# Performance work log

Measured on AMD Instinct MI355X. Metric: run time of the kernel, lower is better.

## Reference

```python
import jax, jax.numpy as jnp
import numpy as np

DIM = 512
NUM_HEADS = 8
HEAD_DIM = DIM // NUM_HEADS
EPS = 1e-12  # F.normalize default eps


def _l2norm(x):
    # F.normalize: x / max(||x||_2, eps) along last dim
    n = jnp.sqrt(jnp.sum(x * x, axis=-1, keepdims=True))
    return x / jnp.maximum(n, EPS)


def setup_inputs() -> dict:
    key = jax.random.key(0)
    ks = jax.random.split(key, 7)
    B, N, K = 8, 4096, 256
    scale = 1.0 / np.sqrt(DIM)
    return {
        "X_flat": jax.random.normal(ks[0], (B, N, DIM), jnp.float32),
        "S_tokens": jax.random.normal(ks[1], (B, K, DIM), jnp.float32),
        "Wq": jax.random.normal(ks[2], (DIM, DIM), jnp.float32) * scale,
        "Wk": jax.random.normal(ks[3], (DIM, DIM), jnp.float32) * scale,
        "Wv": jax.random.normal(ks[4], (DIM, DIM), jnp.float32) * scale,
        "Wo": jax.random.normal(ks[5], (DIM, DIM), jnp.float32) * scale,
        "temperature": jnp.ones((NUM_HEADS, 1, 1), jnp.float32),
    }


def reference(X_flat, S_tokens, Wq, Wk, Wv, Wo, temperature):
    B, N, C = X_flat.shape
    K = S_tokens.shape[1]
    H, D = NUM_HEADS, HEAD_DIM
    # torch Linear: y = x @ W.T
    q = (X_flat @ Wq.T).reshape(B, N, H, D).transpose(0, 2, 1, 3)   # (B,H,N,D)
    k = (S_tokens @ Wk.T).reshape(B, K, H, D).transpose(0, 2, 1, 3)  # (B,H,K,D)
    v = (S_tokens @ Wv.T).reshape(B, K, H, D).transpose(0, 2, 1, 3)  # (B,H,K,D)
    q = _l2norm(q)
    k = _l2norm(k)
    attn = jnp.einsum('bhnd,bhkd->bhnk', q, k) * temperature  # temperature (H,1,1) broadcasts
    attn = jax.nn.softmax(attn, axis=-1)
    out = jnp.einsum('bhnk,bhkd->bhnd', attn, v)
    out = out.transpose(0, 2, 1, 3).reshape(B, N, C)
    out = out @ Wo.T
    return X_flat + out
```

## Files before the change

kernel.cpp:

```cpp
#include <hip/hip_runtime.h>
#include <hip/hip_bf16.h>


typedef __bf16 bf16;
typedef __attribute__((ext_vector_type(8))) __bf16 bf16x8;
typedef __attribute__((ext_vector_type(4))) float f32x4;

#if __has_builtin(__builtin_amdgcn_exp2f)
#define EXP2(x) __builtin_amdgcn_exp2f(x)
#else
#define EXP2(x) exp2f(x)
#endif

__device__ __forceinline__ void gload_lds16(const void* g, void* l) {
  __builtin_amdgcn_global_load_lds(
      (__attribute__((address_space(1))) void*)g,
      (__attribute__((address_space(3))) void*)l, 16, 0, 0);
}

__device__ __forceinline__ unsigned pack2(float a, float b) {
  unsigned short x = __builtin_bit_cast(unsigned short, (bf16)a);
  unsigned short y = __builtin_bit_cast(unsigned short, (bf16)b);
  return (unsigned)x | ((unsigned)y << 16);
}

__global__ __launch_bounds__(256) void cvt_all(
    const float* __restrict__ X, const float* __restrict__ S,
    const float* __restrict__ Wq, const float* __restrict__ Wk,
    const float* __restrict__ Wv, const float* __restrict__ Wo,
    bf16* __restrict__ Xb, bf16* __restrict__ Sb, bf16* __restrict__ Wqb,
    bf16* __restrict__ Wkb, bf16* __restrict__ Wvb, bf16* __restrict__ Wob) {
  int i = blockIdx.x * 256 + threadIdx.x;
  const float* src;
  bf16* dst;
  int r;
  if (i < 2097152) {
    src = X; dst = Xb; r = i;
  } else if (i < 2228224) {
    src = S; dst = Sb; r = i - 2097152;
  } else {
    int j = i - 2228224;
    int w = j >> 15;
    r = j & 32767;
    src = (w == 0) ? Wq : (w == 1) ? Wk : (w == 2) ? Wv : Wo;
    dst = (w == 0) ? Wqb : (w == 1) ? Wkb : (w == 2) ? Wvb : Wob;
  }
  float4 a = *(const float4*)(src + (size_t)r * 8);
  float4 b = *(const float4*)(src + (size_t)r * 8 + 4);
  uint4 v;
  v.x = pack2(a.x, a.y);
  v.y = pack2(a.z, a.w);
  v.z = pack2(b.x, b.y);
  v.w = pack2(b.z, b.w);
  *(uint4*)(dst + (size_t)r * 8) = v;
}

__global__ __launch_bounds__(256) void proj_all(
    const bf16* __restrict__ Xb, const bf16* __restrict__ Sb,
    const bf16* __restrict__ Wqb, const bf16* __restrict__ Wkb,
    const bf16* __restrict__ Wvb, const float* __restrict__ temp,
    bf16* __restrict__ Q, bf16* __restrict__ Kn, bf16* __restrict__ Vt) {
  __shared__ __align__(16) char smem[49152];

  const int lg = (blockIdx.x & 7) * 144 + (blockIdx.x >> 3);

  const bf16* A;
  const bf16* W;
  int m0, kind;
  if (lg < 1024) {
    kind = 0; A = Xb; W = Wqb; m0 = (lg >> 2) * 128;
  } else if (lg < 1088) {
    kind = 1; A = Sb; W = Wkb; m0 = ((lg - 1024) >> 2) * 128;
  } else {
    kind = 2; A = Sb; W = Wvb; m0 = ((lg - 1088) >> 2) * 128;
  }
  const int n0 = (lg & 3) * 128;

  const int tid = threadIdx.x;
  const int wid = tid >> 6, lane = tid & 63;
  const int wr = wid >> 1, wc = wid & 1;
  const int g = lane >> 4, c16 = lane & 15;
  const int r0 = tid >> 2, cc0 = tid & 3;
  const int r1 = (256 + tid) >> 2, cc1 = tid & 3;
  const int dst0 = (tid & ~63) * 16, dst1 = (256 + (tid & ~63)) * 16;

  f32x4 acc[4][4] = {};

#define PSTAGE(kb, buf)                                                     \
  {                                                                         \
    char* as = smem + (buf) * 8192;                                         \
    char* bs = smem + 24576 + (buf) * 8192;                                 \
    gload_lds16(A + (size_t)(m0 + r0) * 512 + (kb) + cc0 * 8, as + dst0);   \
    gload_lds16(A + (size_t)(m0 + r1) * 512 + (kb) + cc1 * 8, as + dst1);   \
    gload_lds16(W + (size_t)(n0 + r0) * 512 + (kb) + cc0 * 8, bs + dst0);   \
    gload_lds16(W + (size_t)(n0 + r1) * 512 + (kb) + cc1 * 8, bs + dst1);   \
  }

#define PCOMPUTE(buf)                                                       \
  {                                                                         \
    const bf16* as = (const bf16*)(smem + (buf) * 8192);                    \
    const bf16* bs = (const bf16*)(smem + 24576 + (buf) * 8192);            \
    bf16x8 af[4], bfr[4];                                                   \
    _Pragma("unroll") for (int mi = 0; mi < 4; ++mi) af[mi] =               \
        *(const bf16x8*)(as + (wr * 64 + mi * 16 + c16) * 32 + g * 8);      \
    _Pragma("unroll") for (int ni = 0; ni < 4; ++ni) bfr[ni] =              \
        *(const bf16x8*)(bs + (wc * 64 + ni * 16 + c16) * 32 + g * 8);      \
    _Pragma("unroll") for (int mi = 0; mi < 4; ++mi)                        \
        _Pragma("unroll") for (int ni = 0; ni < 4; ++ni) acc[mi][ni] =      \
            __builtin_amdgcn_mfma_f32_16x16x32_bf16(af[mi], bfr[ni],        \
                                                    acc[mi][ni], 0, 0, 0);  \
  }

  PSTAGE(0, 0);
  PSTAGE(32, 1);
  int bufc = 0;
  for (int t = 0; t < 14; ++t) {
    int bufn = bufc + 2;
    if (bufn >= 3) bufn -= 3;
    PSTAGE((t + 2) * 32, bufn);
    asm volatile("s_waitcnt vmcnt(8)" ::: "memory");
    __builtin_amdgcn_s_barrier();
    PCOMPUTE(bufc);
    __builtin_amdgcn_s_barrier();
    if (++bufc == 3) bufc = 0;
  }
  asm volatile("s_waitcnt vmcnt(4)" ::: "memory");
  __builtin_amdgcn_s_barrier();
  PCOMPUTE(bufc);
  __builtin_amdgcn_s_barrier();
  if (++bufc == 3) bufc = 0;
  asm volatile("s_waitcnt vmcnt(0)" ::: "memory");
  __builtin_amdgcn_s_barrier();
  PCOMPUTE(bufc);

  __syncthreads();

  if (kind != 2) {
    bf16* C = (kind == 0) ? Q : Kn;
    const float sc =
        (kind == 0) ? temp[(n0 + wc * 64) >> 6] * 1.44269504088896f : 1.0f;
    char* eps = smem + wid * 8192;
#pragma unroll
    for (int mi = 0; mi < 4; ++mi) {
      float ss[4];
#pragma unroll
      for (int j = 0; j < 4; ++j) {
        float s = 0.f;
#pragma unroll
        for (int ni = 0; ni < 4; ++ni) {
          float v = acc[mi][ni][j];
          s += v * v;
        }
        ss[j] = s;
      }
#pragma unroll
      for (int msk = 1; msk < 16; msk <<= 1)
#pragma unroll
        for (int j = 0; j < 4; ++j) ss[j] += __shfl_xor(ss[j], msk, 64);
      float inv[4];
#pragma unroll
      for (int j = 0; j < 4; ++j)
        inv[j] = rsqrtf(fmaxf(ss[j], 1e-24f)) * sc;
#pragma unroll
      for (int ni = 0; ni < 4; ++ni)
#pragma unroll
        for (int j = 0; j < 4; ++j) {
          int row = mi * 16 + g * 4 + j, col = ni * 16 + c16;
          int off = (row * 128 + col * 2) ^ ((row & 7) << 4);
          *(bf16*)(eps + off) = (bf16)(acc[mi][ni][j] * inv[j]);
        }
    }
    asm volatile("s_waitcnt lgkmcnt(0)" ::: "memory");
#pragma unroll
    for (int it = 0; it < 8; ++it) {
      int c = it * 64 + lane;
      int row = c >> 3, ch = c & 7;
      int off = (row * 128 + ch * 16) ^ ((row & 7) << 4);
      bf16x8 v = *(const bf16x8*)(eps + off);
      *(bf16x8*)(C + (size_t)(m0 + wr * 64 + row) * 512 + n0 + wc * 64 +
                 ch * 8) = v;
    }
  } else {
#pragma unroll
    for (int mi = 0; mi < 4; ++mi) {
      int m = m0 + wr * 64 + mi * 16 + g * 4;
      int b = m >> 8, tt = m & 255;
#pragma unroll
      for (int ni = 0; ni < 4; ++ni) {
        int col = n0 + wc * 64 + ni * 16 + c16;
        int h = col >> 6, d = col & 63;
        uint2 v;
        v.x = pack2(acc[mi][ni][0], acc[mi][ni][1]);
        v.y = pack2(acc[mi][ni][2], acc[mi][ni][3]);
        *(uint2*)(Vt + ((size_t)((b * 8 + h) * 64 + d) * 256 + tt)) = v;
      }
    }
  }
#undef PSTAGE
#undef PCOMPUTE
}

__global__ __launch_bounds__(256) void out_gemm(
    const bf16* __restrict__ O, const bf16* __restrict__ Wob,
    const float* __restrict__ Xres, float* __restrict__ out) {
  __shared__ __align__(16) char smem[49152];

  const int lg = (blockIdx.x & 7) * 128 + (blockIdx.x >> 3);
  const int m0 = (lg >> 2) * 128, n0 = (lg & 3) * 128;

  const int tid = threadIdx.x;
  const int wid = tid >> 6, lane = tid & 63;
  const int wr = wid >> 1, wc = wid & 1;
  const int g = lane >> 4, c16 = lane & 15;
  const int r0 = tid >> 2, cc0 = tid & 3;
  const int r1 = (256 + tid) >> 2, cc1 = tid & 3;
  const int dst0 = (tid & ~63) * 16, dst1 = (256 + (tid & ~63)) * 16;

  f32x4 acc[4][4] = {};

#define OSTAGE(kb, buf)                                                      \
  {                                                                          \
    char* as = smem + (buf) * 8192;                                          \
    char* bs = smem + 24576 + (buf) * 8192;                                  \
    gload_lds16(O + (size_t)(m0 + r0) * 512 + (kb) + cc0 * 8, as + dst0);    \
    gload_lds16(O + (size_t)(m0 + r1) * 512 + (kb) + cc1 * 8, as + dst1);    \
    gload_lds16(Wob + (size_t)(n0 + r0) * 512 + (kb) + cc0 * 8, bs + dst0);  \
    gload_lds16(Wob + (size_t)(n0 + r1) * 512 + (kb) + cc1 * 8, bs + dst1);  \
  }

#define OCOMPUTE(buf)                                                       \
  {                                                                         \
    const bf16* as = (const bf16*)(smem + (buf) * 8192);                    \
    const bf16* bs = (const bf16*)(smem + 24576 + (buf) * 8192);            \
    bf16x8 af[4], bfr[4];                                                   \
    _Pragma("unroll") for (int mi = 0; mi < 4; ++mi) af[mi] =               \
        *(const bf16x8*)(as + (wr * 64 + mi * 16 + c16) * 32 + g * 8);      \
    _Pragma("unroll") for (int ni = 0; ni < 4; ++ni) bfr[ni] =              \
        *(const bf16x8*)(bs + (wc * 64 + ni * 16 + c16) * 32 + g * 8);      \
    _Pragma("unroll") for (int mi = 0; mi < 4; ++mi)                        \
        _Pragma("unroll") for (int ni = 0; ni < 4; ++ni) acc[mi][ni] =      \
            __builtin_amdgcn_mfma_f32_16x16x32_bf16(af[mi], bfr[ni],        \
                                                    acc[mi][ni], 0, 0, 0);  \
  }

  OSTAGE(0, 0);
  OSTAGE(32, 1);
  int bufc = 0;
  for (int t = 0; t < 14; ++t) {
    int bufn = bufc + 2;
    if (bufn >= 3) bufn -= 3;
    OSTAGE((t + 2) * 32, bufn);
    asm volatile("s_waitcnt vmcnt(8)" ::: "memory");
    __builtin_amdgcn_s_barrier();
    OCOMPUTE(bufc);
    __builtin_amdgcn_s_barrier();
    if (++bufc == 3) bufc = 0;
  }
  asm volatile("s_waitcnt vmcnt(4)" ::: "memory");
  __builtin_amdgcn_s_barrier();
  OCOMPUTE(bufc);
  __builtin_amdgcn_s_barrier();
  if (++bufc == 3) bufc = 0;
  asm volatile("s_waitcnt vmcnt(0)" ::: "memory");
  __builtin_amdgcn_s_barrier();
  OCOMPUTE(bufc);

  __syncthreads();

  char* eps = smem + wid * 8192;
#pragma unroll
  for (int p = 0; p < 2; ++p) {
#pragma unroll
    for (int mm = 0; mm < 2; ++mm)
#pragma unroll
      for (int ni = 0; ni < 4; ++ni)
#pragma unroll
        for (int j = 0; j < 4; ++j) {
          int row = mm * 16 + g * 4 + j, col = ni * 16 + c16;
          int off = (row * 256 + col * 4) ^ ((row & 7) << 4);
          *(float*)(eps + off) = acc[p * 2 + mm][ni][j];
        }
    asm volatile("s_waitcnt lgkmcnt(0)" ::: "memory");
#pragma unroll
    for (int it = 0; it < 8; ++it) {
      int c = it * 64 + lane;
      int row = c >> 4, ch = c & 15;
      int off = (row * 256 + ch * 16) ^ ((row & 7) << 4);
      float4 v = *(const float4*)(eps + off);
      size_t gr = (size_t)(m0 + wr * 64 + p * 32 + row) * 512 + n0 +
                  wc * 64 + ch * 4;
      float4 x = *(const float4*)(Xres + gr);
      v.x += x.x;
      v.y += x.y;
      v.z += x.z;
      v.w += x.w;
      *(float4*)(out + gr) = v;
    }
    asm volatile("s_waitcnt lgkmcnt(0)" ::: "memory");
  }
#undef OSTAGE
#undef OCOMPUTE
}

__global__ __launch_bounds__(256) void attn_fused(
    const bf16* __restrict__ Qn, const bf16* __restrict__ Kn,
    const bf16* __restrict__ Vt, bf16* __restrict__ O) {
  __shared__ __align__(16) char smem[65536];

  const int tid = threadIdx.x;
  const int w = tid >> 6, lane = tid & 63;
  const int g = lane >> 4, c16 = lane & 15;
  const int lg = (blockIdx.x & 7) * 512 + (blockIdx.x >> 3);
  const int nt = lg & 63, h = (lg >> 6) & 7, b = lg >> 9;
  const int n0 = nt * 64;

  {
    const bf16* Ksrc = Kn + ((size_t)b * 256) * 512 + h * 64;
    const bf16* Vsrc = Vt + (size_t)((b * 8 + h) * 64) * 256;
#pragma unroll
    for (int it = 0; it < 8; ++it) {
      int base = it * 256 + w * 64;
      int c = base + lane;
      int ii = c >> 6, rr = c & 63;
      int fc16 = rr & 15, fg = rr >> 4;
      int kmi = ii >> 1, ks_ = ii & 1;
      gload_lds16(Ksrc + (size_t)(kmi * 16 + fc16) * 512 + ks_ * 32 + fg * 8,
                  smem + base * 16);
      int vks = ii >> 2, vni = ii & 3;
      gload_lds16(Vsrc + (size_t)(vni * 16 + fc16) * 256 + vks * 32 + fg * 8,
                  smem + 32768 + base * 16);
    }
  }
  const int q = w * 16 + c16;
  const bf16* Qsrc = Qn + ((size_t)b * 4096 + n0) * 512 + h * 64;
  bf16x8 qf[2];
  qf[0] = *(const bf16x8*)(Qsrc + (size_t)q * 512 + g * 8);
  qf[1] = *(const bf16x8*)(Qsrc + (size_t)q * 512 + 32 + g * 8);
  __syncthreads();

  f32x4 sacc[16] = {};
#pragma unroll
  for (int mi = 0; mi < 16; ++mi) {
#pragma unroll
    for (int s = 0; s < 2; ++s) {
      bf16x8 kf = *(const bf16x8*)(smem + ((mi * 2 + s) * 64 + lane) * 16);
      sacc[mi] = __builtin_amdgcn_mfma_f32_16x16x32_bf16(kf, qf[s], sacc[mi],
                                                         0, 0, 0);
    }
  }

  float mx4[4] = {-1e30f, -1e30f, -1e30f, -1e30f};
#pragma unroll
  for (int mi = 0; mi < 16; ++mi)
#pragma unroll
    for (int j = 0; j < 4; ++j) mx4[j] = fmaxf(mx4[j], sacc[mi][j]);
  float mx = fmaxf(fmaxf(mx4[0], mx4[1]), fmaxf(mx4[2], mx4[3]));
  mx = fmaxf(mx, __shfl_xor(mx, 16, 64));
  mx = fmaxf(mx, __shfl_xor(mx, 32, 64));
  float sm4[4] = {0.f, 0.f, 0.f, 0.f};
#pragma unroll
  for (int mi = 0; mi < 16; ++mi)
#pragma unroll
    for (int j = 0; j < 4; ++j) {
      float p = EXP2(sacc[mi][j] - mx);
      sacc[mi][j] = p;
      sm4[j] += p;
    }
  float sum = (sm4[0] + sm4[1]) + (sm4[2] + sm4[3]);
  sum += __shfl_xor(sum, 16, 64);
  sum += __shfl_xor(sum, 32, 64);
  float inv = 1.0f / sum;

  __syncthreads();

  char* pslice = smem + w * 8192;
#pragma unroll
  for (int mi = 0; mi < 16; ++mi) {
    int un = (mi >> 1) * 64 + ((mi & 1) * 2 + (g >> 1)) * 16 + c16;
    uint2 v;
    v.x = pack2(sacc[mi][0], sacc[mi][1]);
    v.y = pack2(sacc[mi][2], sacc[mi][3]);
    *(uint2*)(pslice + un * 16 + (g & 1) * 8) = v;
  }
  asm volatile("s_waitcnt lgkmcnt(0)" ::: "memory");
  __builtin_amdgcn_sched_barrier(0);

  f32x4 oacc[4] = {};
#pragma unroll
  for (int ks = 0; ks < 8; ++ks) {
    bf16x8 pa = *(const bf16x8*)(pslice + (ks * 64 + lane) * 16);
#pragma unroll
    for (int ni = 0; ni < 4; ++ni) {
      bf16x8 vb =
          *(const bf16x8*)(smem + 32768 + ((ks * 4 + ni) * 64 + lane) * 16);
      oacc[ni] = __builtin_amdgcn_mfma_f32_16x16x32_bf16(pa, vb, oacc[ni],
                                                         0, 0, 0);
    }
  }
  asm volatile("s_waitcnt lgkmcnt(0)" ::: "memory");
  __builtin_amdgcn_sched_barrier(0);

  {
#pragma unroll
    for (int ni = 0; ni < 4; ++ni)
#pragma unroll
      for (int j = 0; j < 4; ++j) {
        int row = g * 4 + j, col = ni * 16 + c16;
        int off = (row * 128 + col * 2) ^ ((row & 7) << 4);
        *(bf16*)(pslice + off) = (bf16)(oacc[ni][j] * inv);
      }
    asm volatile("s_waitcnt lgkmcnt(0)" ::: "memory");
    __builtin_amdgcn_sched_barrier(0);
#pragma unroll
    for (int it = 0; it < 2; ++it) {
      int c = it * 64 + lane;
      int row = c >> 3, ch = c & 7;
      int off = (row * 128 + ch * 16) ^ ((row & 7) << 4);
      bf16x8 v = *(const bf16x8*)(pslice + off);
      *(bf16x8*)(O + ((size_t)b * 4096 + n0 + w * 16 + row) * 512 + h * 64 +
                 ch * 8) = v;
    }
  }
}

extern "C" void kernel_launch(void* const* d_in, const int* in_sizes, int n_in,
                              void* d_out, int out_size, void* d_ws,
                              size_t ws_size, hipStream_t stream) {
  const float* X = (const float*)d_in[0];
  const float* S = (const float*)d_in[1];
  const float* Wq = (const float*)d_in[2];
  const float* Wk = (const float*)d_in[3];
  const float* Wv = (const float*)d_in[4];
  const float* Wo = (const float*)d_in[5];
  const float* temp = (const float*)d_in[6];
  float* out = (float*)d_out;

  char* ws = (char*)d_ws;
  bf16* Qws = (bf16*)ws;
  bf16* Kws = (bf16*)(ws + 33554432);
  bf16* Vtws = (bf16*)(ws + 35651584);
  bf16* Wqb = (bf16*)(ws + 37748736);
  bf16* Wkb = (bf16*)(ws + 38273024);
  bf16* Wvb = (bf16*)(ws + 38797312);
  bf16* Wob = (bf16*)(ws + 39321600);

  bf16* Xb = (bf16*)d_out;
  bf16* Sb = (bf16*)((char*)d_out + 33554432);

  cvt_all<<<dim3(9216), dim3(256), 0, stream>>>(X, S, Wq, Wk, Wv, Wo, Xb, Sb,
                                                Wqb, Wkb, Wvb, Wob);
  proj_all<<<dim3(1152), dim3(256), 0, stream>>>(Xb, Sb, Wqb, Wkb, Wvb, temp,
                                                 Qws, Kws, Vtws);
  attn_fused<<<dim3(4096), dim3(256), 0, stream>>>(Qws, Kws, Vtws, Qws);
  out_gemm<<<dim3(1024), dim3(256), 0, stream>>>(Qws, Wob, X, out);
}
```

Before: 131.8 us.

## Store Q/K/V in MFMA-fragment order so attention loads are contiguous

The projection epilogue now writes Q, K and V straight into per-(batch,head) images laid out in the order the attention kernel's MFMA fragments read them. Attention can then fill LDS with contiguous 16-byte loads, and each Q fragment becomes one coalesced load instead of a strided gather across 512-wide rows. The projection is split into two launches, K/V first and then Q, with Q placed in the output buffer over the S region that phase 1 has already consumed. The extra launch and the more scattered global stores in the epilogue are the cost, and the buffer aliasing only works because of the launch order.

```diff
diff --git a/kernel.cpp b/kernel.cpp
--- a/kernel.cpp
+++ b/kernel.cpp
@@ -55,26 +55,34 @@
   *(uint4*)(dst + (size_t)r * 8) = v;
 }
 
+template <int PHASE>
 __global__ __launch_bounds__(256) void proj_all(
     const bf16* __restrict__ Xb, const bf16* __restrict__ Sb,
     const bf16* __restrict__ Wqb, const bf16* __restrict__ Wkb,
     const bf16* __restrict__ Wvb, const float* __restrict__ temp,
-    bf16* __restrict__ Q, bf16* __restrict__ Kn, bf16* __restrict__ Vt) {
+    bf16* __restrict__ Qf, bf16* __restrict__ Kf, bf16* __restrict__ Vf) {
   __shared__ __align__(16) char smem[49152];
-
-  const int lg = (blockIdx.x & 7) * 144 + (blockIdx.x >> 3);
 
   const bf16* A;
   const bf16* W;
-  int m0, kind;
-  if (lg < 1024) {
-    kind = 0; A = Xb; W = Wqb; m0 = (lg >> 2) * 128;
-  } else if (lg < 1088) {
-    kind = 1; A = Sb; W = Wkb; m0 = ((lg - 1024) >> 2) * 128;
+  int m0, n0, kind;
+  if (PHASE == 0) {
+    const int lg = (blockIdx.x & 7) * 128 + (blockIdx.x >> 3);
+    kind = 0; A = Xb; W = Wqb;
+    m0 = (lg >> 2) * 128;
+    n0 = (lg & 3) * 128;
   } else {
-    kind = 2; A = Sb; W = Wvb; m0 = ((lg - 1088) >> 2) * 128;
-  }
-  const int n0 = (lg & 3) * 128;
+    const int lg = (blockIdx.x & 7) * 16 + (blockIdx.x >> 3);
+    if (lg < 64) {
+      kind = 1; A = Sb; W = Wkb;
+      m0 = (lg >> 2) * 128;
+      n0 = (lg & 3) * 128;
+    } else {
+      kind = 2; A = Sb; W = Wvb;
+      m0 = ((lg - 64) >> 2) * 128;
+      n0 = ((lg - 64) & 3) * 128;
+    }
+  }
 
   const int tid = threadIdx.x;
   const int wid = tid >> 6, lane = tid & 63;
@@ -136,7 +144,6 @@
   __syncthreads();
 
   if (kind != 2) {
-    bf16* C = (kind == 0) ? Q : Kn;
     const float sc =
         (kind == 0) ? temp[(n0 + wc * 64) >> 6] * 1.44269504088896f : 1.0f;
     char* eps = smem + wid * 8192;
@@ -171,28 +178,44 @@
         }
     }
     asm volatile("s_waitcnt lgkmcnt(0)" ::: "memory");
+    __builtin_amdgcn_sched_barrier(0);
 #pragma unroll
     for (int it = 0; it < 8; ++it) {
       int c = it * 64 + lane;
       int row = c >> 3, ch = c & 7;
       int off = (row * 128 + ch * 16) ^ ((row & 7) << 4);
       bf16x8 v = *(const bf16x8*)(eps + off);
-      *(bf16x8*)(C + (size_t)(m0 + wr * 64 + row) * 512 + n0 + wc * 64 +
-                 ch * 8) = v;
+      int rg = m0 + wr * 64 + row;
+      int cg = n0 + wc * 64 + ch * 8;
+      int hh = cg >> 6, d0 = cg & 63;
+      if (kind == 0) {
+        int bb = rg >> 12, qr = rg & 4095;
+        int unit = ((qr >> 4) * 2 + (d0 >> 5)) * 64 + ((d0 & 31) >> 3) * 16 +
+                   (qr & 15);
+        *(bf16x8*)(Qf + (((size_t)(bb * 8 + hh)) << 18) + unit * 8) = v;
+      } else {
+        int bb = rg >> 8, tt = rg & 255;
+        int unit = ((tt >> 4) * 2 + (d0 >> 5)) * 64 + ((d0 & 31) >> 3) * 16 +
+                   (tt & 15);
+        *(bf16x8*)(Kf + (((size_t)(bb * 8 + hh)) << 14) + unit * 8) = v;
+      }
     }
   } else {
 #pragma unroll
     for (int mi = 0; mi < 4; ++mi) {
       int m = m0 + wr * 64 + mi * 16 + g * 4;
-      int b = m >> 8, tt = m & 255;
+      int bb = m >> 8, tt = m & 255;
 #pragma unroll
       for (int ni = 0; ni < 4; ++ni) {
         int col = n0 + wc * 64 + ni * 16 + c16;
-        int h = col >> 6, d = col & 63;
+        int hh = col >> 6, d = col & 63;
+        int unit = ((tt >> 5) * 4 + (d >> 4)) * 64 + ((tt >> 3) & 3) * 16 +
+                   (d & 15);
         uint2 v;
         v.x = pack2(acc[mi][ni][0], acc[mi][ni][1]);
         v.y = pack2(acc[mi][ni][2], acc[mi][ni][3]);
-        *(uint2*)(Vt + ((size_t)((b * 8 + h) * 64 + d) * 256 + tt)) = v;
+        *(uint2*)(Vf + (((size_t)(bb * 8 + hh)) << 14) + unit * 8 +
+                  (tt & 7)) = v;
       }
     }
   }
@@ -281,6 +304,7 @@
           *(float*)(eps + off) = acc[p * 2 + mm][ni][j];
         }
     asm volatile("s_waitcnt lgkmcnt(0)" ::: "memory");
+    __builtin_amdgcn_sched_barrier(0);
 #pragma unroll
     for (int it = 0; it < 8; ++it) {
       int c = it * 64 + lane;
@@ -297,14 +321,15 @@
       *(float4*)(out + gr) = v;
     }
     asm volatile("s_waitcnt lgkmcnt(0)" ::: "memory");
+    __builtin_amdgcn_sched_barrier(0);
   }
 #undef OSTAGE
 #undef OCOMPUTE
 }
 
 __global__ __launch_bounds__(256) void attn_fused(
-    const bf16* __restrict__ Qn, const bf16* __restrict__ Kn,
-    const bf16* __restrict__ Vt, bf16* __restrict__ O) {
+    const bf16* __restrict__ Qf, const bf16* __restrict__ Kf,
+    const bf16* __restrict__ Vf, bf16* __restrict__ O) {
   __shared__ __align__(16) char smem[65536];
 
   const int tid = threadIdx.x;
@@ -314,28 +339,22 @@
   const int nt = lg & 63, h = (lg >> 6) & 7, b = lg >> 9;
   const int n0 = nt * 64;
 
+  const bf16* Kimg = Kf + (((size_t)(b * 8 + h)) << 14);
+  const bf16* Vimg = Vf + (((size_t)(b * 8 + h)) << 14);
+  const bf16* Qimg = Qf + (((size_t)(b * 8 + h)) << 18);
+
+#pragma unroll
+  for (int it = 0; it < 8; ++it) {
+    int base = it * 256 + w * 64;
+    gload_lds16(Kimg + (size_t)(base + lane) * 8, smem + base * 16);
+    gload_lds16(Vimg + (size_t)(base + lane) * 8, smem + 32768 + base * 16);
+  }
+  bf16x8 qf[2];
   {
-    const bf16* Ksrc = Kn + ((size_t)b * 256) * 512 + h * 64;
-    const bf16* Vsrc = Vt + (size_t)((b * 8 + h) * 64) * 256;
-#pragma unroll
-    for (int it = 0; it < 8; ++it) {
-      int base = it * 256 + w * 64;
-      int c = base + lane;
-      int ii = c >> 6, rr = c & 63;
-      int fc16 = rr & 15, fg = rr >> 4;
-      int kmi = ii >> 1, ks_ = ii & 1;
-      gload_lds16(Ksrc + (size_t)(kmi * 16 + fc16) * 512 + ks_ * 32 + fg * 8,
-                  smem + base * 16);
-      int vks = ii >> 2, vni = ii & 3;
-      gload_lds16(Vsrc + (size_t)(vni * 16 + fc16) * 256 + vks * 32 + fg * 8,
-                  smem + 32768 + base * 16);
-    }
-  }
-  const int q = w * 16 + c16;
-  const bf16* Qsrc = Qn + ((size_t)b * 4096 + n0) * 512 + h * 64;
-  bf16x8 qf[2];
-  qf[0] = *(const bf16x8*)(Qsrc + (size_t)q * 512 + g * 8);
-  qf[1] = *(const bf16x8*)(Qsrc + (size_t)q * 512 + 32 + g * 8);
+    int ub = (nt * 4 + w) * 2;
+    qf[0] = *(const bf16x8*)(Qimg + (size_t)((ub + 0) * 64 + lane) * 8);
+    qf[1] = *(const bf16x8*)(Qimg + (size_t)((ub + 1) * 64 + lane) * 8);
+  }
   __syncthreads();
 
   f32x4 sacc[16] = {};
@@ -371,6 +390,7 @@
   sum += __shfl_xor(sum, 32, 64);
   float inv = 1.0f / sum;
 
+  const int q = w * 16 + c16;
   __syncthreads();
 
   char* pslice = smem + w * 8192;
@@ -436,9 +456,9 @@
   float* out = (float*)d_out;
 
   char* ws = (char*)d_ws;
-  bf16* Qws = (bf16*)ws;
-  bf16* Kws = (bf16*)(ws + 33554432);
-  bf16* Vtws = (bf16*)(ws + 35651584);
+  bf16* Ows = (bf16*)ws;
+  bf16* Kf = (bf16*)(ws + 33554432);
+  bf16* Vf = (bf16*)(ws + 35651584);
   bf16* Wqb = (bf16*)(ws + 37748736);
   bf16* Wkb = (bf16*)(ws + 38273024);
   bf16* Wvb = (bf16*)(ws + 38797312);
@@ -446,11 +466,14 @@
 
   bf16* Xb = (bf16*)d_out;
   bf16* Sb = (bf16*)((char*)d_out + 33554432);
+  bf16* Qf = (bf16*)((char*)d_out + 33554432);
 
   cvt_all<<<dim3(9216), dim3(256), 0, stream>>>(X, S, Wq, Wk, Wv, Wo, Xb, Sb,
                                                 Wqb, Wkb, Wvb, Wob);
-  proj_all<<<dim3(1152), dim3(256), 0, stream>>>(Xb, Sb, Wqb, Wkb, Wvb, temp,
-                                                 Qws, Kws, Vtws);
-  attn_fused<<<dim3(4096), dim3(256), 0, stream>>>(Qws, Kws, Vtws, Qws);
-  out_gemm<<<dim3(1024), dim3(256), 0, stream>>>(Qws, Wob, X, out);
-}
+  proj_all<1><<<dim3(128), dim3(256), 0, stream>>>(Xb, Sb, Wqb, Wkb, Wvb,
+                                                   temp, Qf, Kf, Vf);
+  proj_all<0><<<dim3(1024), dim3(256), 0, stream>>>(Xb, Sb, Wqb, Wkb, Wvb,
+                                                    temp, Qf, Kf, Vf);
+  attn_fused<<<dim3(4096), dim3(256), 0, stream>>>(Qf, Kf, Vf, Ows);
+  out_gemm<<<dim3(1024), dim3(256), 0, stream>>>(Ows, Wob, X, out);
+}
```

Result: faster. 127.7 us (-3.1%).
